# Optimization experiments

Hardware: AMD Instinct MI355X
Metric: run time of the kernel (lower is better)

Reference implementation:

```python
import jax, jax.numpy as jnp
import numpy as np

T_ENC = 80
MAX_LEN = 80
B = 64
D_IN = 4096
EU = 1024
DU = 1024
VOCAB = 20000
ATT = 80


def _lstm_scan(xs, h0, c0, W_ih, W_hh, b_ih, b_hh):
    """Single-layer LSTM over leading time dim. xs: [T,B,I]. Returns (ys[T,B,H], hT, cT)."""
    def step(carry, x):
        h, c = carry
        g = x @ W_ih.T + b_ih + h @ W_hh.T + b_hh
        i, f, gg, o = jnp.split(g, 4, axis=-1)
        c = jax.nn.sigmoid(f) * c + jax.nn.sigmoid(i) * jnp.tanh(gg)
        h = jax.nn.sigmoid(o) * jnp.tanh(c)
        return (h, c), h
    (hT, cT), ys = jax.lax.scan(step, (h0, c0), xs)
    return ys, hT, cT


def setup_inputs() -> dict:
    key = jax.random.key(0)
    ks = jax.random.split(key, 20)
    s = 0.05
    inp = {
        "input_data": jax.random.normal(ks[0], (T_ENC, B, D_IN), jnp.float32),
        "correct_answer": jax.random.normal(ks[1], (MAX_LEN, B, VOCAB), jnp.float32),
        # encoder LSTM params (torch gate order i,f,g,o)
        "enc_W_ih": jax.random.normal(ks[2], (4 * EU, D_IN), jnp.float32) * s,
        "enc_W_hh": jax.random.normal(ks[3], (4 * EU, EU), jnp.float32) * s,
        "enc_b_ih": jax.random.normal(ks[4], (4 * EU,), jnp.float32) * s,
        "enc_b_hh": jax.random.normal(ks[5], (4 * EU,), jnp.float32) * s,
        # decoder LSTM: input = decoder_unit + encoder_unit
        "dec_W_ih": jax.random.normal(ks[6], (4 * DU, DU + EU), jnp.float32) * s,
        "dec_W_hh": jax.random.normal(ks[7], (4 * DU, DU), jnp.float32) * s,
        "dec_b_ih": jax.random.normal(ks[8], (4 * DU,), jnp.float32) * s,
        "dec_b_hh": jax.random.normal(ks[9], (4 * DU,), jnp.float32) * s,
        # embeddings
        "in_emb_W": jax.random.normal(ks[10], (DU, VOCAB), jnp.float32) * s,
        "in_emb_b": jax.random.normal(ks[11], (DU,), jnp.float32) * s,
        "out_emb_W": jax.random.normal(ks[12], (VOCAB, DU), jnp.float32) * s,
        "out_emb_b": jax.random.normal(ks[13], (VOCAB,), jnp.float32) * s,
        # attention: linear_l1du_max ((d_l+1)*d_u -> 80), linear_2du_du (2*d_u -> d_u)
        "att_W1": jax.random.normal(ks[14], (ATT, 2 * DU), jnp.float32) * s,
        "att_b1": jax.random.normal(ks[15], (ATT,), jnp.float32) * s,
        "att_W2": jax.random.normal(ks[16], (DU, 2 * DU), jnp.float32) * s,
        "att_b2": jax.random.normal(ks[17], (DU,), jnp.float32) * s,
        "prelu_w": jnp.full((1,), 0.25, jnp.float32),  # PReLU(num_parameters=1) init
        "max_len": 80,
        "real_ans_length": jax.random.randint(ks[18], (B,), 0, 80),
    }
    return inp


def reference(input_data, correct_answer,
              enc_W_ih, enc_W_hh, enc_b_ih, enc_b_hh,
              dec_W_ih, dec_W_hh, dec_b_ih, dec_b_hh,
              in_emb_W, in_emb_b, out_emb_W, out_emb_b,
              att_W1, att_b1, att_W2, att_b2, prelu_w,
              max_len, real_ans_length):
    z_eh = jnp.zeros((B, EU), jnp.float32)
    z_dh = jnp.zeros((B, DU), jnp.float32)

    # encoding stage
    enc_seq, enc_h, enc_c = _lstm_scan(input_data, z_eh, z_eh, enc_W_ih, enc_W_hh, enc_b_ih, enc_b_hh)
    pad_tag = jnp.zeros((input_data.shape[0], B, DU), jnp.float32)
    dec_in0 = jnp.concatenate([enc_seq, pad_tag], axis=2)
    dec_out_seq, dec_h, dec_c = _lstm_scan(dec_in0, z_dh, z_dh, dec_W_ih, dec_W_hh, dec_b_ih, dec_b_hh)

    # encoder over zero padding inputs (continues encoder state)
    pad_in = jnp.zeros((max_len, B, D_IN), jnp.float32)
    enc_pad_seq, _, _ = _lstm_scan(pad_in, enc_h, enc_c, enc_W_ih, enc_W_hh, enc_b_ih, enc_b_hh)

    # teacher-forced samples (schedule_sample_rate == 1 -> always ground truth)
    bos = jnp.zeros((B, VOCAB), jnp.float32).at[:, -2].set(1.0)
    sample0 = bos @ in_emb_W.T + in_emb_b                              # [B, DU]
    samples_rest = correct_answer[1:max_len] @ in_emb_W.T + in_emb_b  # [max_len-1, B, DU]
    samples = jnp.concatenate([sample0[None], samples_rest], axis=0)   # [max_len, B, DU]

    E = enc_seq  # [80, B, EU]; attention weights have exactly 80 slots

    def dec_step(carry, inp):
        h, c = carry
        sample, enc_pad = inp
        # Attention: i = h (single layer), a = concat(i, word)
        a = jnp.concatenate([h, sample], axis=-1)          # [B, 2*DU]
        w = jax.nn.softmax(a @ att_W1.T + att_b1, axis=1)  # [B, 80]
        f = jnp.einsum('bs,sbh->bh', w, E)                 # [B, EU]
        cc = jnp.concatenate([sample, f], axis=-1)         # [B, 2*DU]
        z = cc @ att_W2.T + att_b2
        o = jnp.where(z >= 0, z, prelu_w[0] * z)           # PReLU (scalar param)
        context = o + enc_pad                              # [B, EU]
        x = jnp.concatenate([sample, context], axis=-1)    # [B, DU+EU]
        g = x @ dec_W_ih.T + dec_b_ih + h @ dec_W_hh.T + dec_b_hh
        gi, gf, gg, go = jnp.split(g, 4, axis=-1)
        c = jax.nn.sigmoid(gf) * c + jax.nn.sigmoid(gi) * jnp.tanh(gg)
        h = jax.nn.sigmoid(go) * jnp.tanh(c)
        word = h @ out_emb_W.T + out_emb_b                 # [B, VOCAB]
        return (h, c), word

    (_, _), words = jax.lax.scan(dec_step, (dec_h, dec_c), (samples, enc_pad_seq))
    return words  # [max_len, B, VOCAB]
```

## Files before the change

### kernel.cpp

```cpp
#include <hip/hip_runtime.h>
#include <cstddef>
#include <cstdint>

typedef __attribute__((ext_vector_type(8))) short short8v;
typedef __attribute__((ext_vector_type(4))) float f32x4;

__device__ __forceinline__ float sigmf(float x) { return 1.0f / (1.0f + __expf(-x)); }

__device__ __forceinline__ unsigned short bf16_rn(float x) {
    union { float f; unsigned u; } v; v.f = x;
    unsigned r = v.u + 0x7FFF + ((v.u >> 16) & 1);
    return (unsigned short)(r >> 16);
}
__device__ __forceinline__ float bf16_to_f(unsigned short h) {
    union { unsigned u; float f; } v; v.u = ((unsigned)h) << 16; return v.f;
}
__device__ __forceinline__ unsigned long long pack4(unsigned short a, unsigned short b,
                                                    unsigned short c, unsigned short d) {
    return (unsigned long long)a | ((unsigned long long)b << 16)
         | ((unsigned long long)c << 32) | ((unsigned long long)d << 48);
}

#define MFMA_(d, va, vb) d = __builtin_amdgcn_mfma_f32_16x16x32_bf16(va, vb, d, 0, 0, 0)

#define AT_LD(p)        __hip_atomic_load((p), __ATOMIC_RELAXED, __HIP_MEMORY_SCOPE_AGENT)
#define AT_ST(p, v)     __hip_atomic_store((p), (v), __ATOMIC_RELAXED, __HIP_MEMORY_SCOPE_AGENT)
#define AT_ST_REL(p, v) __hip_atomic_store((p), (v), __ATOMIC_RELEASE, __HIP_MEMORY_SCOPE_AGENT)
#define AT_ADD(p, v)    __hip_atomic_fetch_add((p), (v), __ATOMIC_RELAXED, __HIP_MEMORY_SCOPE_AGENT)

__device__ __forceinline__ void write_frag3_nt(unsigned short* __restrict__ dst, int NRGW,
                                               int r, int k, float x)
{
    unsigned short hi = bf16_rn(x); float r1 = x - bf16_to_f(hi);
    unsigned short md = bf16_rn(r1);
    unsigned short lo = bf16_rn(r1 - bf16_to_f(md));
    int base = (((r >> 4) * 32 + (k >> 5)) * 64 + ((k >> 3) & 3) * 16 + (r & 15)) * 8 + (k & 7);
    int ps = NRGW * 16384;
    __builtin_nontemporal_store(hi, &dst[base]);
    __builtin_nontemporal_store(md, &dst[ps + base]);
    __builtin_nontemporal_store(lo, &dst[2 * ps + base]);
}

__launch_bounds__(256)
__global__ void rearr_frag(const float* __restrict__ src, int ld, int c0,
                           unsigned short* __restrict__ dst, int R, int K)
{
    int idx = blockIdx.x * 256 + threadIdx.x;
    int kpr = K >> 3;
    if (idx >= R * kpr) return;
    int r = idx / kpr, k = (idx % kpr) * 8;
    int NRGW = R >> 4;
    const float* s = src + (size_t)r * ld + c0 + k;
    float4 v0 = *(const float4*)s, v1 = *(const float4*)(s + 4);
    float xs[8] = {v0.x, v0.y, v0.z, v0.w, v1.x, v1.y, v1.z, v1.w};
    unsigned short hi[8], md[8], lo[8];
#pragma unroll
    for (int e = 0; e < 8; ++e) {
        hi[e] = bf16_rn(xs[e]); float r1 = xs[e] - bf16_to_f(hi[e]);
        md[e] = bf16_rn(r1);
        lo[e] = bf16_rn(r1 - bf16_to_f(md[e]));
    }
    int base = (((r >> 4) * 32 + (k >> 5)) * 64 + ((k >> 3) & 3) * 16 + (r & 15)) * 8;
    size_t ps = (size_t)NRGW * 16384;
    *(unsigned long long*)&dst[base]          = pack4(hi[0], hi[1], hi[2], hi[3]);
    *(unsigned long long*)&dst[base + 4]      = pack4(hi[4], hi[5], hi[6], hi[7]);
    *(unsigned long long*)&dst[ps + base]     = pack4(md[0], md[1], md[2], md[3]);
    *(unsigned long long*)&dst[ps + base + 4] = pack4(md[4], md[5], md[6], md[7]);
    *(unsigned long long*)&dst[2*ps + base]     = pack4(lo[0], lo[1], lo[2], lo[3]);
    *(unsigned long long*)&dst[2*ps + base + 4] = pack4(lo[4], lo[5], lo[6], lo[7]);
}

__device__ __forceinline__ void tree_barrier(unsigned* bar, int gidx, int ng, int bpg)
{
    __syncthreads();
    if (threadIdx.x == 0) {
        unsigned* gcnt = bar + gidx * 32;
        unsigned* ggen = bar + gidx * 32 + 1;
        unsigned* rcnt = bar + ng * 32;
        unsigned* rgen = bar + ng * 32 + 1;
        __threadfence();
        unsigned mygen = AT_LD(ggen);
        unsigned prev = AT_ADD(gcnt, 1u);
        if (prev == (unsigned)(bpg - 1)) {
            AT_ST(gcnt, 0u);
            unsigned rg = AT_LD(rgen);
            unsigned rprev = AT_ADD(rcnt, 1u);
            if (rprev == (unsigned)(ng - 1)) {
                AT_ST(rcnt, 0u);
                AT_ST_REL(rgen, rg + 1u);
            } else {
                while (AT_LD(rgen) == rg) __builtin_amdgcn_s_sleep(1);
            }
            AT_ST_REL(ggen, mygen + 1u);
        } else {
            while (AT_LD(ggen) == mygen) __builtin_amdgcn_s_sleep(1);
        }
        __threadfence();
    }
    __syncthreads();
}

template <int NS>
__launch_bounds__(256, 2)
__global__ void gemm_mfma_split(const float* __restrict__ A, int lda,
                                const float* __restrict__ W, int ldw,
                                float* __restrict__ C, int ldc,
                                const float* __restrict__ bias,
                                int M, int N, int K)
{
    __shared__ unsigned short Abf[NS][128][40];
    __shared__ unsigned short Bbf[NS][128][40];
    const int tid = threadIdx.x;
    const int m0 = blockIdx.y * 128, n0 = blockIdx.x * 128;
    const int wave = tid >> 6, lane = tid & 63;
    const int wr = wave >> 1, wc = wave & 1;
    const int lr = lane & 15, lk = (lane >> 4) * 8;

    f32x4 acc[4][4];
#pragma unroll
    for (int i = 0; i < 4; ++i)
#pragma unroll
        for (int j = 0; j < 4; ++j) acc[i][j] = (f32x4){0.f, 0.f, 0.f, 0.f};

    const int arow = tid >> 1;
    const int akh  = (tid & 1) * 16;
    int gr = m0 + arow; if (gr > M - 1) gr = M - 1;
    int gn = n0 + arow; if (gn > N - 1) gn = N - 1;
    const float* aptr = A + (size_t)gr * lda + akh;
    const float* wptr = W + (size_t)gn * ldw + akh;

    for (int k0 = 0; k0 < K; k0 += 32) {
#pragma unroll
        for (int q = 0; q < 4; ++q) {
            float4 v = *(const float4*)(aptr + k0 + q * 4);
            float xs[4] = {v.x, v.y, v.z, v.w};
            unsigned short h[4], hm[4], hl[4];
#pragma unroll
            for (int e = 0; e < 4; ++e) {
                h[e] = bf16_rn(xs[e]);
                if (NS == 3) {
                    float r1 = xs[e] - bf16_to_f(h[e]);
                    hm[e] = bf16_rn(r1);
                    hl[e] = bf16_rn(r1 - bf16_to_f(hm[e]));
                }
            }
            *(unsigned long long*)&Abf[0][arow][akh + q * 4] = pack4(h[0], h[1], h[2], h[3]);
            if (NS == 3) {
                *(unsigned long long*)&Abf[1][arow][akh + q * 4] = pack4(hm[0], hm[1], hm[2], hm[3]);
                *(unsigned long long*)&Abf[2][arow][akh + q * 4] = pack4(hl[0], hl[1], hl[2], hl[3]);
            }
        }
#pragma unroll
        for (int q = 0; q < 4; ++q) {
            float4 v = *(const float4*)(wptr + k0 + q * 4);
            float xs[4] = {v.x, v.y, v.z, v.w};
            unsigned short h[4], hm[4], hl[4];
#pragma unroll
            for (int e = 0; e < 4; ++e) {
                h[e] = bf16_rn(xs[e]);
                if (NS == 3) {
                    float r1 = xs[e] - bf16_to_f(h[e]);
                    hm[e] = bf16_rn(r1);
                    hl[e] = bf16_rn(r1 - bf16_to_f(hm[e]));
                }
            }
            *(unsigned long long*)&Bbf[0][arow][akh + q * 4] = pack4(h[0], h[1], h[2], h[3]);
            if (NS == 3) {
                *(unsigned long long*)&Bbf[1][arow][akh + q * 4] = pack4(hm[0], hm[1], hm[2], hm[3]);
                *(unsigned long long*)&Bbf[2][arow][akh + q * 4] = pack4(hl[0], hl[1], hl[2], hl[3]);
            }
        }
        __syncthreads();

        short8v a[NS][4], b[4];
#pragma unroll
        for (int p = 0; p < NS; ++p)
#pragma unroll
            for (int i = 0; i < 4; ++i)
                a[p][i] = *(const short8v*)&Abf[p][wr * 64 + i * 16 + lr][lk];
#pragma unroll
        for (int q = 0; q < NS; ++q) {
#pragma unroll
            for (int j = 0; j < 4; ++j)
                b[j] = *(const short8v*)&Bbf[q][wc * 64 + j * 16 + lr][lk];
            const int pmax = (NS == 1) ? 1 : (3 - q);
#pragma unroll
            for (int p = 0; p < 3; ++p) {
                if (p >= pmax) break;
#pragma unroll
                for (int i = 0; i < 4; ++i)
#pragma unroll
                    for (int j = 0; j < 4; ++j)
                        acc[i][j] = __builtin_amdgcn_mfma_f32_16x16x32_bf16(
                            a[p][i], b[j], acc[i][j], 0, 0, 0);
            }
        }
        __syncthreads();
    }

    const int crow = (lane >> 4) * 4;
#pragma unroll
    for (int i = 0; i < 4; ++i) {
        int mbase = m0 + wr * 64 + i * 16 + crow;
#pragma unroll
        for (int j = 0; j < 4; ++j) {
            int n = n0 + wc * 64 + j * 16 + lr;
            if (n < N) {
                float bv = bias[n];
#pragma unroll
                for (int r = 0; r < 4; ++r) {
                    int m = mbase + r;
                    if (m < M) C[(size_t)m * ldc + n] = acc[i][j][r] + bv;
                }
            }
        }
    }
}

__launch_bounds__(256)
__global__ void zero_f(float* __restrict__ p, int n)
{
    int i = blockIdx.x * 256 + threadIdx.x;
    if (i < n) p[i] = 0.f;
}

__launch_bounds__(256)
__global__ void vec_add2(const float* __restrict__ a, const float* __restrict__ b,
                         float* __restrict__ o, int n)
{
    int i = blockIdx.x * 256 + threadIdx.x;
    if (i < n) o[i] = a[i] + b[i];
}

__launch_bounds__(256)
__global__ void sample0_fill(const float* __restrict__ emW, const float* __restrict__ emb,
                             float* __restrict__ samples)
{
    int idx = blockIdx.x * 256 + threadIdx.x;
    int d = idx & 1023;
    samples[idx] = emW[(size_t)d * 20000 + 19998] + emb[d];
}

__device__ __forceinline__ void stage_A(unsigned short* __restrict__ LDSA,
                                        const unsigned short* __restrict__ src,
                                        int rg, int tid)
{
#pragma unroll
    for (int p = 0; p < 3; ++p) {
        const unsigned short* sp = src + (size_t)(p * 4 + rg) * 16384;
        unsigned short* dp = LDSA + p * 16384;
#pragma unroll
        for (int it = 0; it < 4; ++it) {
            int idx = tid + it * 512;
            *(short8v*)&dp[idx * 8] = *(const short8v*)&sp[idx * 8];
        }
    }
}

__device__ __forceinline__ f32x4 mfma16(const unsigned short* __restrict__ LDSA,
                                        const short8v* __restrict__ wreg,
                                        int kh, int lane)
{
    f32x4 acc0 = (f32x4){0.f,0.f,0.f,0.f}, acc1 = acc0;
#pragma unroll
    for (int i = 0; i < 16; ++i) {
        int kf = kh * 16 + i;
        short8v a0 = *(const short8v*)&LDSA[(kf * 64 + lane) * 8];
        short8v a1 = *(const short8v*)&LDSA[16384 + (kf * 64 + lane) * 8];
        short8v a2 = *(const short8v*)&LDSA[32768 + (kf * 64 + lane) * 8];
        short8v b0 = wreg[i * 3 + 0], b1 = wreg[i * 3 + 1], b2 = wreg[i * 3 + 2];
        f32x4& A = (i & 1) ? acc1 : acc0;
        MFMA_(A, a0, b0); MFMA_(A, a0, b1); MFMA_(A, a1, b0);
        MFMA_(A, a1, b1); MFMA_(A, a0, b2); MFMA_(A, a2, b0);
    }
    return acc0 + acc1;
}

__launch_bounds__(512, 1)
__global__ void coop_enc80(const unsigned short* __restrict__ WencF,
                           const float* __restrict__ Xbig,
                           unsigned short* __restrict__ hfrag,
                           float* __restrict__ enc_seq,
                           float* __restrict__ cglobE,
                           unsigned* __restrict__ bar)
{
    __shared__ unsigned short LDSA[3 * 16384];
    __shared__ float gbuf[8][16][16];
    const int bid = blockIdx.x, tid = threadIdx.x;
    const int w = tid >> 6, lane = tid & 63;
    const int g = w & 3, kh = w >> 2;
    const int rg = bid >> 6, cg = bid & 63;
    const int wbase = g * 64 + cg;
    const int r_l = (tid & 255) >> 4, c_l = tid & 15;
    const int row = rg * 16 + r_l, col = cg * 16 + c_l;
    float cstate = 0.f;

    short8v wreg[48];
#pragma unroll
    for (int i = 0; i < 16; ++i) {
        int kf = kh * 16 + i;
#pragma unroll
        for (int p = 0; p < 3; ++p)
            wreg[i * 3 + p] = *(const short8v*)&WencF[((size_t)(p * 256 + wbase) * 32 + kf) * 512 + lane * 8];
    }

    float pf[4];
    if (tid < 256) {
#pragma unroll
        for (int g2 = 0; g2 < 4; ++g2)
            pf[g2] = Xbig[(size_t)row * 4096 + g2 * 1024 + col];
    }

    for (int s = 0; s < 80; ++s) {
        const unsigned short* hf = hfrag + (s & 1) * 196608;
        stage_A(LDSA, hf, rg, tid);
        __syncthreads();
        f32x4 acc = mfma16(LDSA, wreg, kh, lane);
#pragma unroll
        for (int r = 0; r < 4; ++r)
            gbuf[w][(lane >> 4) * 4 + r][lane & 15] = acc[r];
        __syncthreads();

        if (tid < 256) {
            float gv[4];
#pragma unroll
            for (int g2 = 0; g2 < 4; ++g2)
                gv[g2] = gbuf[g2][r_l][c_l] + gbuf[4 + g2][r_l][c_l] + pf[g2];
            float cn = sigmf(gv[1]) * cstate + sigmf(gv[0]) * tanhf(gv[2]);
            float hn = sigmf(gv[3]) * tanhf(cn);
            cstate = cn;
            __builtin_nontemporal_store(hn, &enc_seq[(size_t)s * 65536 + row * 1024 + col]);
            write_frag3_nt(hfrag + ((s + 1) & 1) * 196608, 4, row, col, hn);
            if (s == 79) __builtin_nontemporal_store(cstate, &cglobE[row * 1024 + col]);
            else {
#pragma unroll
                for (int g2 = 0; g2 < 4; ++g2)
                    pf[g2] = Xbig[((size_t)(s + 1) * 64 + row) * 4096 + g2 * 1024 + col];
            }
        }
        tree_barrier(bar, bid >> 5, 8, 32);
    }
}

__launch_bounds__(512, 1)
__global__ void coop_padwarm(const unsigned short* __restrict__ WencF,
                             const unsigned short* __restrict__ WdecF,
                             const float* __restrict__ benc,
                             const float* __restrict__ Xwarm,
                             const float* __restrict__ cglobE,
                             unsigned short* __restrict__ hfragE,
                             unsigned short* __restrict__ hfragD,
                             float* __restrict__ enc_pad,
                             float* __restrict__ cglobD,
                             float* __restrict__ h_fp32,
                             unsigned* __restrict__ barE,
                             unsigned* __restrict__ barW)
{
    __shared__ unsigned short LDSA[3 * 16384];
    __shared__ float gbuf[8][16][16];
    const int bid = blockIdx.x, tid = threadIdx.x;
    const int w = tid >> 6, lane = tid & 63;
    const int g = w & 3, kh = w >> 2;
    const bool isW = bid >= 128;
    const int lb = bid & 127;
    const int rg2 = lb >> 6, cg = lb & 63;
    const int wbase = g * 64 + cg;
    const int r_l = (tid & 255) >> 4, c_l = tid & 15;
    const int col = cg * 16 + c_l;
    const unsigned short* Wf = isW ? WdecF : WencF;
    unsigned short* hfrag = isW ? hfragD : hfragE;
    unsigned* bar = isW ? barW : barE;

    short8v wreg[48];
#pragma unroll
    for (int i = 0; i < 16; ++i) {
        int kf = kh * 16 + i;
#pragma unroll
        for (int p = 0; p < 3; ++p)
            wreg[i * 3 + p] = *(const short8v*)&Wf[((size_t)(p * 256 + wbase) * 32 + kf) * 512 + lane * 8];
    }

    float cst[2] = {0.f, 0.f};
    float pfx[2][4];
    if (tid < 256) {
#pragma unroll
        for (int l = 0; l < 2; ++l) {
            int row = rg2 * 32 + l * 16 + r_l;
            if (!isW) cst[l] = cglobE[row * 1024 + col];
#pragma unroll
            for (int g2 = 0; g2 < 4; ++g2)
                pfx[l][g2] = isW ? Xwarm[(size_t)row * 4096 + g2 * 1024 + col]
                                 : benc[g2 * 1024 + col];
        }
    }

    for (int s = 0; s < 80; ++s) {
        const unsigned short* hf = hfrag + (s & 1) * 196608;
        unsigned short* hout = hfrag + ((s + 1) & 1) * 196608;
#pragma unroll
        for (int l = 0; l < 2; ++l) {
            const int rgi = rg2 * 2 + l;
            stage_A(LDSA, hf, rgi, tid);
            __syncthreads();
            f32x4 acc = mfma16(LDSA, wreg, kh, lane);
#pragma unroll
            for (int r = 0; r < 4; ++r)
                gbuf[w][(lane >> 4) * 4 + r][lane & 15] = acc[r];
            __syncthreads();
            if (tid < 256) {
                const int row = rgi * 16 + r_l;
                float gv[4];
#pragma unroll
                for (int g2 = 0; g2 < 4; ++g2)
                    gv[g2] = gbuf[g2][r_l][c_l] + gbuf[4 + g2][r_l][c_l] + pfx[l][g2];
                float cn = sigmf(gv[1]) * cst[l] + sigmf(gv[0]) * tanhf(gv[2]);
                float hn = sigmf(gv[3]) * tanhf(cn);
                cst[l] = cn;
                if (!isW)
                    __builtin_nontemporal_store(hn, &enc_pad[(size_t)s * 65536 + row * 1024 + col]);
                write_frag3_nt(hout, 4, row, col, hn);
                if (isW) {
                    if (s == 79) {
                        __builtin_nontemporal_store(hn, &h_fp32[row * 1024 + col]);
                        __builtin_nontemporal_store(cn, &cglobD[row * 1024 + col]);
                    } else {
#pragma unroll
                        for (int g2 = 0; g2 < 4; ++g2)
                            pfx[l][g2] = Xwarm[((size_t)(s + 1) * 64 + row) * 4096 + g2 * 1024 + col];
                    }
                }
            }
            __syncthreads();
        }
        tree_barrier(bar, (lb >> 5), 4, 32);
    }
}

__launch_bounds__(512, 2)
__global__ void coop_dec80(const unsigned short* __restrict__ WihcF,
                           const unsigned short* __restrict__ WhhF,
                           const float* __restrict__ W1,
                           const float* __restrict__ EW2,
                           const float* __restrict__ S_g,
                           const float* __restrict__ ctxS,
                           const float* __restrict__ S_log,
                           const float* __restrict__ enc_pad,
                           const float* __restrict__ prelu_w,
                           const float* __restrict__ h_fp32,
                           const float* __restrict__ cglobD,
                           unsigned short* __restrict__ hfrag,
                           unsigned short* __restrict__ ctxfrag,
                           float* __restrict__ plog,
                           float* __restrict__ h_all,
                           float* __restrict__ gsum,
                           unsigned* __restrict__ bar)
{
    __shared__ float EW2T[80 * 256];
    __shared__ float gred[8][1024];
    __shared__ float hq[256];
    __shared__ float wsm[80];
    __shared__ float rbuf[128];
    const int bid = blockIdx.x, tid = threadIdx.x;
    const int w = tid >> 6, lane = tid & 63;
    const int gg = bid >> 6, cg = bid & 63;
    const int wbase = gg * 64 + cg;
    const int kq = w;
    const int b = bid >> 2, jc = bid & 3;
    const float pw = prelu_w[0];

    const unsigned short* Wsrc = (kq < 4) ? WihcF : WhhF;
    const int kfbase = (kq & 3) * 8;
    short8v wreg[24];
#pragma unroll
    for (int i = 0; i < 8; ++i) {
#pragma unroll
        for (int p = 0; p < 3; ++p)
            wreg[i * 3 + p] = *(const short8v*)&Wsrc[((size_t)(p * 256 + wbase) * 32 + kfbase + i) * 512 + lane * 8];
    }

    float cstate = (tid < 256) ? cglobD[b * 1024 + jc * 256 + tid] : 0.f;

    for (int i = tid; i < 80 * 256; i += 512) {
        int ss = i >> 8, j = i & 255;
        EW2T[i] = EW2[((size_t)ss * 64 + b) * 1024 + jc * 256 + j];
    }
    __syncthreads();

    for (int s = 80; s < 160; ++s) {
        unsigned short* hout = hfrag + ((s + 1) & 1) * 196608;
        const unsigned short* hf = hfrag + (s & 1) * 196608;
        const int t = s - 80;

        if (s == 80) {
            float* hsm_ = (float*)gred;
            for (int i = tid; i < 1024; i += 512) hsm_[i] = h_fp32[b * 1024 + i];
            __syncthreads();
#pragma unroll
            for (int i = 0; i < 10; ++i) {
                int sx = w * 10 + i;
                float p = 0.f;
#pragma unroll
                for (int q = 0; q < 16; ++q)
                    p = fmaf(hsm_[lane + q * 64], W1[(size_t)sx * 2048 + lane + q * 64], p);
#pragma unroll
                for (int off = 32; off; off >>= 1) p += __shfl_down(p, off, 64);
                if (lane == 0) wsm[sx] = p + S_log[((size_t)t * 64 + b) * 80 + sx];
            }
            __syncthreads();
        } else {
            if (tid < 80) {
                float l4 = plog[(b * 4 + 0) * 80 + tid] + plog[(b * 4 + 1) * 80 + tid]
                         + plog[(b * 4 + 2) * 80 + tid] + plog[(b * 4 + 3) * 80 + tid];
                wsm[tid] = l4 + S_log[((size_t)t * 64 + b) * 80 + tid];
            }
            __syncthreads();
        }
        float v = (tid < 80) ? wsm[tid] : -3.4e38f;
        if (tid < 128) rbuf[tid] = v;
        __syncthreads();
        for (int off = 64; off >= 1; off >>= 1) {
            if (tid < off) rbuf[tid] = fmaxf(rbuf[tid], rbuf[tid + off]);
            __syncthreads();
        }
        float mx = rbuf[0];
        __syncthreads();
        float e = (tid < 80) ? __expf(wsm[tid] - mx) : 0.f;
        if (tid < 128) rbuf[tid] = e;
        __syncthreads();
        for (int off = 64; off >= 1; off >>= 1) {
            if (tid < off) rbuf[tid] += rbuf[tid + off];
            __syncthreads();
        }
        float inv = 1.f / rbuf[0];
        __syncthreads();
        if (tid < 80) wsm[tid] = e * inv;
        __syncthreads();
        if (tid < 256) {
            float f = 0.f;
#pragma unroll 8
            for (int ss = 0; ss < 80; ++ss)
                f = fmaf(wsm[ss], EW2T[ss * 256 + tid], f);
            int col = jc * 256 + tid;
            float val = f + ctxS[((size_t)t * 64 + b) * 1024 + col];
            val = (val >= 0.f) ? val : pw * val;
            val += enc_pad[((size_t)t * 64 + b) * 1024 + col];
            write_frag3_nt(ctxfrag, 4, b, col, val);
        }
        tree_barrier(bar, bid >> 5, 8, 32);

        float pf[4];
        if (tid < 256) {
            const float* xb = S_g + ((size_t)t * 64 + b) * 4096;
            int col = jc * 256 + tid;
#pragma unroll
            for (int g2 = 0; g2 < 4; ++g2) pf[g2] = xb[g2 * 1024 + col];
        }

        {
            f32x4 acc[4];
#pragma unroll
            for (int rg = 0; rg < 4; ++rg) acc[rg] = (f32x4){0.f,0.f,0.f,0.f};
            const unsigned short* asrc = (kq < 4) ? ctxfrag : hf;
#pragma unroll
            for (int i = 0; i < 8; ++i) {
                int kfl = kfbase + i;
#pragma unroll
                for (int rg = 0; rg < 4; ++rg) {
                    const unsigned short* ab = asrc + ((size_t)rg * 32 + kfl) * 512 + lane * 8;
                    short8v a0 = *(const short8v*)&ab[0];
                    short8v a1 = *(const short8v*)&ab[65536];
                    short8v a2 = *(const short8v*)&ab[131072];
                    short8v b0 = wreg[i * 3 + 0], b1 = wreg[i * 3 + 1], b2 = wreg[i * 3 + 2];
                    MFMA_(acc[rg], a0, b0); MFMA_(acc[rg], a0, b1); MFMA_(acc[rg], a1, b0);
                    MFMA_(acc[rg], a1, b1); MFMA_(acc[rg], a0, b2); MFMA_(acc[rg], a2, b0);
                }
            }
#pragma unroll
            for (int rg = 0; rg < 4; ++rg)
#pragma unroll
                for (int r = 0; r < 4; ++r)
                    gred[w][rg * 256 + lane * 4 + r] = acc[rg][r];
            __syncthreads();
#pragma unroll
            for (int e2 = 0; e2 < 2; ++e2) {
                int slot = tid * 2 + e2;
                int rg = slot >> 8, l = (slot >> 2) & 63, r = slot & 3;
                float sum = 0.f;
#pragma unroll
                for (int w2 = 0; w2 < 8; ++w2) sum += gred[w2][slot];
                int row = rg * 16 + (l >> 4) * 4 + r;
                int col = cg * 16 + (l & 15);
                __builtin_nontemporal_store(sum, &gsum[((size_t)gg * 64 + row) * 1024 + col]);
            }
        }
        tree_barrier(bar, bid >> 5, 8, 32);

        if (tid < 256) {
            int col = jc * 256 + tid;
            float gv[4];
#pragma unroll
            for (int g2 = 0; g2 < 4; ++g2)
                gv[g2] = gsum[((size_t)g2 * 64 + b) * 1024 + col] + pf[g2];
            float cn = sigmf(gv[1]) * cstate + sigmf(gv[0]) * tanhf(gv[2]);
            float hn = sigmf(gv[3]) * tanhf(cn);
            cstate = cn;
            __builtin_nontemporal_store(hn, &h_all[((size_t)t * 64 + b) * 1024 + col]);
            write_frag3_nt(hout, 4, b, col, hn);
            hq[tid] = hn;
        }
        __syncthreads();
        if (s < 159) {
#pragma unroll
            for (int i = 0; i < 10; ++i) {
                int sx = w * 10 + i;
                float p = 0.f;
#pragma unroll
                for (int q = 0; q < 4; ++q)
                    p = fmaf(hq[lane + q * 64], W1[(size_t)sx * 2048 + jc * 256 + lane + q * 64], p);
#pragma unroll
                for (int off = 32; off; off >>= 1) p += __shfl_down(p, off, 64);
                if (lane == 0) __builtin_nontemporal_store(p, &plog[(b * 4 + jc) * 80 + sx]);
            }
        }
        tree_barrier(bar, bid >> 5, 8, 32);
    }
}

extern "C" void kernel_launch(void* const* d_in, const int* in_sizes, int n_in,
                              void* d_out, int out_size, void* d_ws, size_t ws_size,
                              hipStream_t stream)
{
    (void)in_sizes; (void)n_in; (void)out_size; (void)ws_size;

    const float* input_data     = (const float*)d_in[0];
    const float* correct_answer = (const float*)d_in[1];
    const float* enc_W_ih = (const float*)d_in[2];
    const float* enc_W_hh = (const float*)d_in[3];
    const float* enc_b_ih = (const float*)d_in[4];
    const float* enc_b_hh = (const float*)d_in[5];
    const float* dec_W_ih = (const float*)d_in[6];
    const float* dec_W_hh = (const float*)d_in[7];
    const float* dec_b_ih = (const float*)d_in[8];
    const float* dec_b_hh = (const float*)d_in[9];
    const float* in_emb_W = (const float*)d_in[10];
    const float* in_emb_b = (const float*)d_in[11];
    const float* out_emb_W = (const float*)d_in[12];
    const float* out_emb_b = (const float*)d_in[13];
    const float* att_W1 = (const float*)d_in[14];
    const float* att_b1 = (const float*)d_in[15];
    const float* att_W2 = (const float*)d_in[16];
    const float* att_b2 = (const float*)d_in[17];
    const float* prelu_w = (const float*)d_in[18];

    float* out = (float*)d_out;
    char* ws = (char*)d_ws;

    float* Xbig    = out;
    float* S_g     = out + 20971520;
    float* ctxS    = out + 41943040;
    float* S_log   = out + 47185920;
    float* samples = out + 47595520;
    float* EW2     = out + 52838400;
    unsigned short* WencF = (unsigned short*)(out + 58081280);
    unsigned short* WhhDF = (unsigned short*)(out + 64372736);
    unsigned short* WihcF = (unsigned short*)(out + 70664192);

    size_t off = 0;
    auto alloc = [&](size_t nfloats) { float* p = (float*)(ws + off); off += nfloats * 4; return p; };
    float* enc_seq = alloc(80 * 64 * 1024);
    float* enc_pad = alloc(80 * 64 * 1024);
    float* h_all   = alloc(80 * 64 * 1024);
    float* benc    = alloc(4096);
    float* bdec    = alloc(4096);
    float* zb      = alloc(1024);
    float* hfragE_f = alloc(196608);
    float* hfragD_f = alloc(196608);
    float* ctxfrag_f= alloc(98304);
    float* plog     = alloc(64 * 4 * 80);
    float* gsum     = alloc(262144);
    float* cglobE   = alloc(65536);
    float* cglobD   = alloc(65536);
    float* h_fp32   = alloc(65536);
    float* bar_f    = alloc(2048);
    unsigned short* hfragE  = (unsigned short*)hfragE_f;
    unsigned short* hfragD  = (unsigned short*)hfragD_f;
    unsigned short* ctxfrag = (unsigned short*)ctxfrag_f;
    unsigned* barE1 = (unsigned*)bar_f;
    unsigned* barPE = ((unsigned*)bar_f) + 512;
    unsigned* barPW = ((unsigned*)bar_f) + 1024;
    unsigned* barD  = ((unsigned*)bar_f) + 1536;

    auto big3 = [&](const float* A, int lda, const float* W, int ldw,
                    float* C, int ldc, const float* bias, int M, int N, int K) {
        dim3 g((N + 127) / 128, (M + 127) / 128);
        hipLaunchKernelGGL((gemm_mfma_split<3>), g, dim3(256), 0, stream,
                           A, lda, W, ldw, C, ldc, bias, M, N, K);
    };

    hipLaunchKernelGGL(vec_add2, dim3(16), dim3(256), 0, stream, enc_b_ih, enc_b_hh, benc, 4096);
    hipLaunchKernelGGL(vec_add2, dim3(16), dim3(256), 0, stream, dec_b_ih, dec_b_hh, bdec, 4096);
    hipLaunchKernelGGL(zero_f, dim3(4), dim3(256), 0, stream, zb, 1024);
    hipLaunchKernelGGL(zero_f, dim3(768), dim3(256), 0, stream, hfragE_f, 196608);
    hipLaunchKernelGGL(zero_f, dim3(768), dim3(256), 0, stream, hfragD_f, 196608);
    hipLaunchKernelGGL(zero_f, dim3(8), dim3(256), 0, stream, bar_f, 2048);

    hipLaunchKernelGGL(rearr_frag, dim3(2048), dim3(256), 0, stream, enc_W_hh, 1024, 0, WencF, 4096, 1024);
    hipLaunchKernelGGL(rearr_frag, dim3(2048), dim3(256), 0, stream, dec_W_hh, 1024, 0, WhhDF, 4096, 1024);
    hipLaunchKernelGGL(rearr_frag, dim3(2048), dim3(256), 0, stream, dec_W_ih, 2048, 1024, WihcF, 4096, 1024);

    big3(input_data, 4096, enc_W_ih, 4096, Xbig, 4096, benc, 5120, 4096, 4096);
    hipLaunchKernelGGL(sample0_fill, dim3(256), dim3(256), 0, stream, in_emb_W, in_emb_b, samples);
    big3(correct_answer + (size_t)64 * 20000, 20000, in_emb_W, 20000,
         samples + 65536, 1024, in_emb_b, 5056, 1024, 20000);
    big3(samples, 1024, dec_W_ih, 2048, S_g, 4096, bdec, 5120, 4096, 1024);
    big3(samples, 1024, att_W2, 2048, ctxS, 1024, att_b2, 5120, 1024, 1024);
    big3(samples, 1024, att_W1 + 1024, 2048, S_log, 80, att_b1, 5120, 80, 1024);

    hipLaunchKernelGGL(coop_enc80, dim3(256), dim3(512), 0, stream,
                       WencF, Xbig, hfragE, enc_seq, cglobE, barE1);

    big3(enc_seq, 1024, dec_W_ih, 2048, Xbig, 4096, bdec, 5120, 4096, 1024);
    big3(enc_seq, 1024, att_W2 + 1024, 2048, EW2, 1024, zb, 5120, 1024, 1024);

    hipLaunchKernelGGL(coop_padwarm, dim3(256), dim3(512), 0, stream,
                       WencF, WhhDF, benc, Xbig, cglobE,
                       hfragE, hfragD, enc_pad, cglobD, h_fp32, barPE, barPW);

    hipLaunchKernelGGL(coop_dec80, dim3(256), dim3(512), 0, stream,
                       WihcF, WhhDF, att_W1, EW2, S_g, ctxS, S_log,
                       enc_pad, prelu_w, h_fp32, cglobD,
                       hfragD, ctxfrag, plog, h_all, gsum, barD);

    {
        dim3 g((20000 + 127) / 128, (5120 + 127) / 128);
        hipLaunchKernelGGL((gemm_mfma_split<1>), g, dim3(256), 0, stream,
                           h_all, 1024, out_emb_W, 1024, out, 20000, out_emb_b, 5120, 20000, 1024);
    }
}
```

Baseline: 15.00 ms.

## Retile decoder gate GEMM to 2x2 row/column tiles and remap block indices

The decoder step GEMM now gives each block two row groups and two 16-column weight tiles instead of four row groups and one column tile. Each loaded A fragment is reused across two weight tiles, which halves activation fragment loads per MFMA. The cost is doubling register-resident weights to 48 vectors, so launch bounds drop to one block per SM. The encoder and warm kernels also remap block ids so adjacent blocks share a column group rather than a row group, changing locality and barrier grouping.

```diff
diff --git a/kernel.cpp b/kernel.cpp
--- a/kernel.cpp
+++ b/kernel.cpp
@@ -289,7 +289,7 @@
     const int bid = blockIdx.x, tid = threadIdx.x;
     const int w = tid >> 6, lane = tid & 63;
     const int g = w & 3, kh = w >> 2;
-    const int rg = bid >> 6, cg = bid & 63;
+    const int rg = bid & 3, cg = bid >> 2;
     const int wbase = g * 64 + cg;
     const int r_l = (tid & 255) >> 4, c_l = tid & 15;
     const int row = rg * 16 + r_l, col = cg * 16 + c_l;
@@ -363,7 +363,7 @@
     const int g = w & 3, kh = w >> 2;
     const bool isW = bid >= 128;
     const int lb = bid & 127;
-    const int rg2 = lb >> 6, cg = lb & 63;
+    const int rg2 = lb & 1, cg = lb >> 1;
     const int wbase = g * 64 + cg;
     const int r_l = (tid & 255) >> 4, c_l = tid & 15;
     const int col = cg * 16 + c_l;
@@ -436,7 +436,7 @@
     }
 }
 
-__launch_bounds__(512, 2)
+__launch_bounds__(512, 1)
 __global__ void coop_dec80(const unsigned short* __restrict__ WihcF,
                            const unsigned short* __restrict__ WhhF,
                            const float* __restrict__ W1,
@@ -462,20 +462,24 @@
     __shared__ float rbuf[128];
     const int bid = blockIdx.x, tid = threadIdx.x;
     const int w = tid >> 6, lane = tid & 63;
-    const int gg = bid >> 6, cg = bid & 63;
-    const int wbase = gg * 64 + cg;
+    const int rp = bid & 1, u = bid >> 1;
     const int kq = w;
     const int b = bid >> 2, jc = bid & 3;
     const float pw = prelu_w[0];
 
     const unsigned short* Wsrc = (kq < 4) ? WihcF : WhhF;
     const int kfbase = (kq & 3) * 8;
-    short8v wreg[24];
-#pragma unroll
-    for (int i = 0; i < 8; ++i) {
-#pragma unroll
-        for (int p = 0; p < 3; ++p)
-            wreg[i * 3 + p] = *(const short8v*)&Wsrc[((size_t)(p * 256 + wbase) * 32 + kfbase + i) * 512 + lane * 8];
+    short8v wreg[48];
+#pragma unroll
+    for (int ct = 0; ct < 2; ++ct) {
+        const int wbase2 = u * 2 + ct;
+#pragma unroll
+        for (int i = 0; i < 8; ++i) {
+#pragma unroll
+            for (int p = 0; p < 3; ++p)
+                wreg[(ct * 8 + i) * 3 + p] =
+                    *(const short8v*)&Wsrc[((size_t)(p * 256 + wbase2) * 32 + kfbase + i) * 512 + lane * 8];
+        }
     }
 
     float cstate = (tid < 256) ? cglobD[b * 1024 + jc * 256 + tid] : 0.f;
@@ -557,40 +561,53 @@
         }
 
         {
-            f32x4 acc[4];
-#pragma unroll
-            for (int rg = 0; rg < 4; ++rg) acc[rg] = (f32x4){0.f,0.f,0.f,0.f};
+            f32x4 acc[2][2];
+#pragma unroll
+            for (int rgl = 0; rgl < 2; ++rgl)
+#pragma unroll
+                for (int ct = 0; ct < 2; ++ct) acc[rgl][ct] = (f32x4){0.f,0.f,0.f,0.f};
             const unsigned short* asrc = (kq < 4) ? ctxfrag : hf;
 #pragma unroll
             for (int i = 0; i < 8; ++i) {
                 int kfl = kfbase + i;
 #pragma unroll
-                for (int rg = 0; rg < 4; ++rg) {
+                for (int rgl = 0; rgl < 2; ++rgl) {
+                    const int rg = rp * 2 + rgl;
                     const unsigned short* ab = asrc + ((size_t)rg * 32 + kfl) * 512 + lane * 8;
                     short8v a0 = *(const short8v*)&ab[0];
                     short8v a1 = *(const short8v*)&ab[65536];
                     short8v a2 = *(const short8v*)&ab[131072];
-                    short8v b0 = wreg[i * 3 + 0], b1 = wreg[i * 3 + 1], b2 = wreg[i * 3 + 2];
-                    MFMA_(acc[rg], a0, b0); MFMA_(acc[rg], a0, b1); MFMA_(acc[rg], a1, b0);
-                    MFMA_(acc[rg], a1, b1); MFMA_(acc[rg], a0, b2); MFMA_(acc[rg], a2, b0);
+#pragma unroll
+                    for (int ct = 0; ct < 2; ++ct) {
+                        short8v b0 = wreg[(ct * 8 + i) * 3 + 0];
+                        short8v b1 = wreg[(ct * 8 + i) * 3 + 1];
+                        short8v b2 = wreg[(ct * 8 + i) * 3 + 2];
+                        MFMA_(acc[rgl][ct], a0, b0); MFMA_(acc[rgl][ct], a0, b1);
+                        MFMA_(acc[rgl][ct], a1, b0); MFMA_(acc[rgl][ct], a1, b1);
+                        MFMA_(acc[rgl][ct], a0, b2); MFMA_(acc[rgl][ct], a2, b0);
+                    }
                 }
             }
 #pragma unroll
-            for (int rg = 0; rg < 4; ++rg)
-#pragma unroll
-                for (int r = 0; r < 4; ++r)
-                    gred[w][rg * 256 + lane * 4 + r] = acc[rg][r];
+            for (int rgl = 0; rgl < 2; ++rgl)
+#pragma unroll
+                for (int ct = 0; ct < 2; ++ct)
+#pragma unroll
+                    for (int r = 0; r < 4; ++r)
+                        gred[w][(rgl * 2 + ct) * 256 + lane * 4 + r] = acc[rgl][ct][r];
             __syncthreads();
 #pragma unroll
             for (int e2 = 0; e2 < 2; ++e2) {
                 int slot = tid * 2 + e2;
-                int rg = slot >> 8, l = (slot >> 2) & 63, r = slot & 3;
+                int t4 = slot >> 8, l = (slot >> 2) & 63, r = slot & 3;
                 float sum = 0.f;
 #pragma unroll
                 for (int w2 = 0; w2 < 8; ++w2) sum += gred[w2][slot];
-                int row = rg * 16 + (l >> 4) * 4 + r;
-                int col = cg * 16 + (l & 15);
-                __builtin_nontemporal_store(sum, &gsum[((size_t)gg * 64 + row) * 1024 + col]);
+                int rgl = t4 >> 1, ct = t4 & 1;
+                int row = rp * 32 + rgl * 16 + (l >> 4) * 4 + r;
+                int fr = (u * 2 + ct) * 16 + (l & 15);
+                __builtin_nontemporal_store(sum,
+                    &gsum[((size_t)(fr >> 10) * 64 + row) * 1024 + (fr & 1023)]);
             }
         }
         tree_barrier(bar, bid >> 5, 8, 32);
```

After: 14.97 ms. About the same (-0.2%).
